# Kernel optimization log

Measured on AMD Instinct MI355X. Metric: run time of the kernel, lower is better.

Reference implementation:

```python
import jax, jax.numpy as jnp
import numpy as np

B, L, D, H, NLAYERS = 32, 2048, 1024, 16, 4
HD = D // H
NEG = -1e30


def setup_inputs() -> dict:
    key = jax.random.key(0)
    ks = jax.random.split(key, 12)
    tokens = jax.random.normal(ks[0], (B, L, D), dtype=jnp.float32)
    lengths = jax.random.randint(ks[1], (B,), 1, L + 1, dtype=jnp.int32)
    query_token = jax.random.normal(ks[2], (1, D), dtype=jnp.float32)
    s = 0.02
    Wq = jax.random.normal(ks[3], (NLAYERS, D, D), dtype=jnp.float32) * s
    Wk = jax.random.normal(ks[4], (NLAYERS, D, D), dtype=jnp.float32) * s
    Wv = jax.random.normal(ks[5], (NLAYERS, D, D), dtype=jnp.float32) * s
    Wo = jax.random.normal(ks[6], (NLAYERS, D, D), dtype=jnp.float32) * s
    bq = jnp.zeros((NLAYERS, D), jnp.float32)
    bk = jnp.zeros((NLAYERS, D), jnp.float32)
    bv = jnp.zeros((NLAYERS, D), jnp.float32)
    bo = jnp.zeros((NLAYERS, D), jnp.float32)
    gamma = jnp.ones((NLAYERS, D), jnp.float32)
    beta = jnp.zeros((NLAYERS, D), jnp.float32)
    return dict(tokens=tokens, lengths=lengths, query_token=query_token,
                Wq=Wq, bq=bq, Wk=Wk, bk=bk, Wv=Wv, bv=bv, Wo=Wo, bo=bo,
                gamma=gamma, beta=beta)


def _layernorm(x, g, b):
    mu = jnp.mean(x, axis=-1, keepdims=True)
    var = jnp.mean(jnp.square(x - mu), axis=-1, keepdims=True)
    return (x - mu) * jax.lax.rsqrt(var + 1e-5) * g + b


def reference(tokens, lengths, query_token, Wq, bq, Wk, bk, Wv, bv, Wo, bo, gamma, beta):
    # valid[b, l] = True where token l exists (inverse of key_padding_mask)
    valid = jnp.arange(L)[None, :] < lengths[:, None]            # [B, L]
    scale = 1.0 / jnp.sqrt(jnp.float32(HD))
    # zero out padded positions like the torch padded buffer (math-neutral)
    toks = tokens * valid[:, :, None].astype(tokens.dtype)       # [B, L, D]
    q = jnp.broadcast_to(query_token[None], (B, 1, D))           # [B, 1, D]
    for i in range(NLAYERS):
        qh = (q @ Wq[i] + bq[i]).reshape(B, 1, H, HD)            # [B, 1, H, hd]
        kh = (toks @ Wk[i] + bk[i]).reshape(B, L, H, HD)         # [B, L, H, hd]
        vh = (toks @ Wv[i] + bv[i]).reshape(B, L, H, HD)
        scores = jnp.einsum('bqhd,bkhd->bhqk', qh, kh) * scale   # [B, H, 1, L]
        scores = jnp.where(valid[:, None, None, :], scores, NEG)
        attn = jax.nn.softmax(scores, axis=-1)
        out = jnp.einsum('bhqk,bkhd->bqhd', attn, vh).reshape(B, 1, D)
        out = out @ Wo[i] + bo[i]
        q = _layernorm(out, gamma[i], beta[i])
    return q[:, 0, :]                                            # [B, D]
```

## Files before the change

### kernel.cpp

```cpp
#include <hip/hip_runtime.h>
#include <hip/hip_bf16.h>
#include <cstdint>
#include <cstddef>

#define BB 32
#define LL 2048
#define DD 1024
#define HH 16
#define HDIM 64
#define NL 4
#define NCHUNK 8
#define CHUNK 256
#define NEGINF -1e30f
#define PKS 16

typedef __attribute__((ext_vector_type(8))) short bf16x8;
typedef __attribute__((ext_vector_type(4))) float f32x4;

__device__ __forceinline__ unsigned short f2b(float x) {
    union { float f; unsigned int u; } v; v.f = x;
    unsigned int r = (v.u + 0x7FFFu + ((v.u >> 16) & 1u)) >> 16;
    return (unsigned short)r;
}
__device__ __forceinline__ float b2f(unsigned short u) {
    union { unsigned int u; float f; } v; v.u = ((unsigned int)u) << 16;
    return v.f;
}

template<int SRC>
__global__ __launch_bounds__(512) void k_gemv(
        const float* __restrict__ parts_in, const float* __restrict__ bias_in,
        const unsigned short* __restrict__ ctx16, const float* __restrict__ m_p,
        const float* __restrict__ s_p,
        const float* __restrict__ W, float* __restrict__ outp) {
    constexpr int KL = DD / PKS;
    int bid = blockIdx.x, tid = threadIdx.x;
    int ct = bid & 15, ks = bid >> 4;
    int e0 = ks * KL;
    __shared__ float Xs[BB][KL];
    __shared__ float wgtS[BB][NCHUNK];
    __shared__ float mgS[BB], SgS[BB];
    if (SRC == 3) {
        if (tid < BB) {
            int b = tid; float m = NEGINF;
            for (int c8 = 0; c8 < NCHUNK; ++c8)
                m = fmaxf(m, m_p[(b * NCHUNK + c8) * HH + ct]);
            float S = 0.f;
            for (int c8 = 0; c8 < NCHUNK; ++c8)
                S += s_p[(b * NCHUNK + c8) * HH + ct] *
                     __expf(m_p[(b * NCHUNK + c8) * HH + ct] - m);
            mgS[b] = m; SgS[b] = S;
        }
        __syncthreads();
        if (tid < 256) {
            int b = tid >> 3, c8 = tid & 7;
            wgtS[b][c8] = __expf(m_p[(b * NCHUNK + c8) * HH + ct] - mgS[b]) / SgS[b];
        }
        __syncthreads();
    }
    {
        int b = tid >> 4, kq = tid & 15;
        int k = kq * 4;
        float x0, x1, x2, x3;
        if (SRC == 2) {
            const float4 bi = *(const float4*)&bias_in[e0 + k];
            x0 = bi.x; x1 = bi.y; x2 = bi.z; x3 = bi.w;
#pragma unroll
            for (int j2 = 0; j2 < PKS; ++j2) {
                const float4 v = *(const float4*)&parts_in[((size_t)(j2 * BB) + b) * DD + e0 + k];
                x0 += v.x; x1 += v.y; x2 += v.z; x3 += v.w;
            }
        } else {
            x0 = x1 = x2 = x3 = 0.f;
#pragma unroll
            for (int c8 = 0; c8 < NCHUNK; ++c8) {
                const ushort4 u = *(const ushort4*)&ctx16[(((size_t)(b * NCHUNK + c8)) * HH + ct) * DD + e0 + k];
                float wq = wgtS[b][c8];
                x0 += wq * b2f(u.x); x1 += wq * b2f(u.y);
                x2 += wq * b2f(u.z); x3 += wq * b2f(u.w);
            }
        }
        float4 xv = {x0, x1, x2, x3};
        *(float4*)&Xs[b][k] = xv;
    }
    __syncthreads();
    int col = tid & 63, bg = tid >> 6;
    int c = ct * 64 + col;
    float acc[4] = {0.f, 0.f, 0.f, 0.f};
    for (int k = 0; k < KL; k += 4) {
        float w0 = W[(size_t)(e0 + k) * DD + c];
        float w1 = W[(size_t)(e0 + k + 1) * DD + c];
        float w2 = W[(size_t)(e0 + k + 2) * DD + c];
        float w3 = W[(size_t)(e0 + k + 3) * DD + c];
#pragma unroll
        for (int bb = 0; bb < 4; ++bb) {
            const float4 xv = *(const float4*)&Xs[bg * 4 + bb][k];
            acc[bb] += xv.x * w0 + xv.y * w1 + xv.z * w2 + xv.w * w3;
        }
    }
#pragma unroll
    for (int bb = 0; bb < 4; ++bb)
        outp[((size_t)(ks * BB) + bg * 4 + bb) * DD + c] = acc[bb];
}

__global__ __launch_bounds__(1024) void k_statsF(const float* __restrict__ parts,
        const float* __restrict__ bo, const float* __restrict__ gamma,
        const float* __restrict__ beta, float* __restrict__ outp) {
    int b = blockIdx.x, c = threadIdx.x;
    float v = bo[c];
#pragma unroll
    for (int ks = 0; ks < PKS; ++ks)
        v += parts[((size_t)(ks * BB) + b) * DD + c];
    float s1 = v, s2 = v * v;
#pragma unroll
    for (int off = 32; off; off >>= 1) {
        s1 += __shfl_xor(s1, off);
        s2 += __shfl_xor(s2, off);
    }
    __shared__ float r1[16], r2[16];
    __shared__ float smu, srs;
    int w = c >> 6;
    if ((c & 63) == 0) { r1[w] = s1; r2[w] = s2; }
    __syncthreads();
    if (c == 0) {
        float a = 0.f, q = 0.f;
#pragma unroll
        for (int i = 0; i < 16; ++i) { a += r1[i]; q += r2[i]; }
        float mu = a / (float)DD, var = q / (float)DD - mu * mu;
        smu = mu; srs = rsqrtf(var + 1e-5f);
    }
    __syncthreads();
    outp[(size_t)b * DD + c] = (v - smu) * srs * gamma[c] + beta[c];
}

__global__ __launch_bounds__(512) void k_qnext(const float* __restrict__ op,
        const float* __restrict__ bo, const float* __restrict__ gamma,
        const float* __restrict__ beta, const float* __restrict__ Wq,
        const float* __restrict__ bq, float* __restrict__ qh) {
    int bid = blockIdx.x, tid = threadIdx.x;
    int ct = bid & 15, bp = bid >> 4;
    int b0 = bp * 2;
    __shared__ float Xr[2][DD];
    __shared__ float pr[8][2][64];
    __shared__ float r1[8], r2[8];
    __shared__ float smu[2], srs[2];
    {
        int bb = tid >> 8, c4 = tid & 255;
        int c = c4 * 4;
        float4 x = *(const float4*)&bo[c];
#pragma unroll
        for (int ks = 0; ks < PKS; ++ks) {
            const float4 v = *(const float4*)&op[((size_t)(ks * BB) + b0 + bb) * DD + c];
            x.x += v.x; x.y += v.y; x.z += v.z; x.w += v.w;
        }
        *(float4*)&Xr[bb][c] = x;
    }
    __syncthreads();
    {
        int bb = tid >> 8, l = tid & 255;
        const float4 x = *(const float4*)&Xr[bb][l * 4];
        float s1 = x.x + x.y + x.z + x.w;
        float s2 = x.x * x.x + x.y * x.y + x.z * x.z + x.w * x.w;
#pragma unroll
        for (int off = 32; off; off >>= 1) {
            s1 += __shfl_xor(s1, off);
            s2 += __shfl_xor(s2, off);
        }
        int w = tid >> 6;
        if ((tid & 63) == 0) { r1[w] = s1; r2[w] = s2; }
    }
    __syncthreads();
    if (tid < 2) {
        float a = r1[tid * 4] + r1[tid * 4 + 1] + r1[tid * 4 + 2] + r1[tid * 4 + 3];
        float q = r2[tid * 4] + r2[tid * 4 + 1] + r2[tid * 4 + 2] + r2[tid * 4 + 3];
        float mu = a / (float)DD, var = q / (float)DD - mu * mu;
        smu[tid] = mu; srs[tid] = rsqrtf(var + 1e-5f);
    }
    __syncthreads();
    {
        int c = tid & 63, ks8 = tid >> 6;
        float mu0 = smu[0], rs0 = srs[0], mu1 = smu[1], rs1 = srs[1];
        float acc0 = 0.f, acc1 = 0.f;
        int k0 = ks8 * 128;
        for (int k = k0; k < k0 + 128; ++k) {
            float g = gamma[k], be = beta[k];
            float w = Wq[(size_t)k * DD + ct * 64 + c];
            float x0 = (Xr[0][k] - mu0) * rs0 * g + be;
            float x1 = (Xr[1][k] - mu1) * rs1 * g + be;
            acc0 += x0 * w;
            acc1 += x1 * w;
        }
        pr[ks8][0][c] = acc0;
        pr[ks8][1][c] = acc1;
    }
    __syncthreads();
    if (tid < 128) {
        int bb = tid >> 6, c = tid & 63;
        float q = bq[ct * 64 + c];
#pragma unroll
        for (int j = 0; j < 8; ++j) q += pr[j][bb][c];
        qh[((size_t)(b0 + bb)) * DD + ct * 64 + c] = q;
    }
}

__global__ __launch_bounds__(256) void k_q0(const float* __restrict__ qt,
        const float* __restrict__ Wq, const float* __restrict__ bq,
        float* __restrict__ qh) {
    int ct = blockIdx.x, tid = threadIdx.x;
    __shared__ float pr[4][64];
    int c = tid & 63, ks4 = tid >> 6;
    float acc = 0.f;
    int k0 = ks4 * 256;
    for (int k = k0; k < k0 + 256; ++k)
        acc += qt[k] * Wq[(size_t)k * DD + ct * 64 + c];
    pr[ks4][c] = acc;
    __syncthreads();
    if (tid < 64) {
        float q = bq[ct * 64 + tid];
#pragma unroll
        for (int j = 0; j < 4; ++j) q += pr[j][tid];
        qh[ct * 64 + tid] = q;
    }
}

template<int BCAST>
__global__ __launch_bounds__(256) void k_wk(const float* __restrict__ qh,
        const float* __restrict__ Wk, const float* __restrict__ bk,
        unsigned short* __restrict__ wk16, float* __restrict__ sb) {
    int h = blockIdx.x >> 4, et = blockIdx.x & 15;
    int tid = threadIdx.x;
    __shared__ float qs[BB][HDIM + 1];
    for (int i = tid; i < BB * HDIM; i += 256) {
        int bb = i >> 6, d = i & 63;
        qs[bb][d] = qh[((size_t)(BCAST ? 0 : bb)) * DD + h * HDIM + d];
    }
    __syncthreads();
    int b = tid & 31, eo = tid >> 5;
    for (int k = 0; k < 8; ++k) {
        int e = et * 64 + eo * 8 + k;
        const float* wrow = Wk + (size_t)e * DD + h * HDIM;
        float acc = 0.f;
#pragma unroll
        for (int d = 0; d < HDIM; ++d) acc += qs[b][d] * wrow[d];
        wk16[((size_t)(b * HH + h)) * DD + e] = f2b(acc);
    }
    if (et == 0 && tid < BB) {
        float acc = 0.f;
#pragma unroll
        for (int d = 0; d < HDIM; ++d) acc += qs[tid][d] * bk[h * HDIM + d];
        sb[tid * HH + h] = acc;
    }
}

template<int MODE>
__global__ __launch_bounds__(1024) void k_attn(const float* __restrict__ toks,
        unsigned short* __restrict__ tcache,
        const int* __restrict__ lens, const unsigned short* __restrict__ wk16,
        const float* __restrict__ sb, unsigned short* __restrict__ ctx16,
        float* __restrict__ m_p, float* __restrict__ s_p) {
    int b = blockIdx.x >> 3, chunk = blockIdx.x & 7;
    int tid = threadIdx.x, lane = tid & 63, w = tid >> 6;
    int len = lens[b];
    int base = chunk * CHUNK;
    int pidx = (b * NCHUNK + chunk) * HH;
    if (base >= len) {
        if (tid < HH) { m_p[pidx + tid] = NEGINF; s_p[pidx + tid] = 0.f; }
        return;
    }
    int nv = min(CHUNK, len - base);

    __shared__ __align__(16) unsigned short Tr[32][1032];
    __shared__ float Sred[16][HH][34];
    __shared__ unsigned short Pt[HH][40];
    __shared__ float sm_m[HH], sm_s[HH], sm_c[HH];

    if (tid < HH) { sm_m[tid] = NEGINF; sm_s[tid] = 0.f; }

    int hq = lane & 15, qg = lane >> 4;
    const unsigned short* wkb = wk16 + ((size_t)(b * HH + hq)) * DD + w * 64 + 8 * qg;
    bf16x8 afr0 = *(const bf16x8*)(wkb);
    bf16x8 afr1 = *(const bf16x8*)(wkb + 32);
    f32x4 zer = {0.f, 0.f, 0.f, 0.f};
    f32x4 ctxacc[4] = {zer, zer, zer, zer};
    float sbh = (tid < 512) ? sb[b * HH + (tid >> 5)] : 0.f;
    int st = tid >> 7;
    int se = (tid & 127) * 8;
    const size_t rowbase = (size_t)(b * LL + base);
    __syncthreads();

    for (int g = 0; g < 8; ++g) {
        int t0 = g * 32;
        if (t0 >= nv) break;
        if (MODE == 2) {
            const unsigned short* srcr = tcache + (rowbase + t0) * DD;
#pragma unroll
            for (int p = 0; p < 4; ++p) {
                int t = p * 8 + st;
                bf16x8 v = *(const bf16x8*)(srcr + (size_t)t * DD + se);
                *(bf16x8*)&Tr[t][se] = v;
            }
        } else {
            const float* srcr = toks + (rowbase + t0) * DD;
#pragma unroll
            for (int p = 0; p < 4; ++p) {
                int t = p * 8 + st;
                const float* sp = srcr + (size_t)t * DD + se;
                float4 a0 = *(const float4*)sp;
                float4 a1 = *(const float4*)(sp + 4);
                bf16x8 v;
                v[0] = f2b(a0.x); v[1] = f2b(a0.y); v[2] = f2b(a0.z); v[3] = f2b(a0.w);
                v[4] = f2b(a1.x); v[5] = f2b(a1.y); v[6] = f2b(a1.z); v[7] = f2b(a1.w);
                *(bf16x8*)&Tr[t][se] = v;
                if (MODE == 1)
                    *(bf16x8*)(tcache + (rowbase + t0 + t) * DD + se) = v;
            }
        }
        __syncthreads();
        f32x4 s0 = zer, s1 = zer;
        {
            int eb = w * 64 + 8 * qg;
            s0 = __builtin_amdgcn_mfma_f32_16x16x32_bf16(afr0, *(const bf16x8*)&Tr[hq][eb], s0, 0, 0, 0);
            s0 = __builtin_amdgcn_mfma_f32_16x16x32_bf16(afr1, *(const bf16x8*)&Tr[hq][eb + 32], s0, 0, 0, 0);
            s1 = __builtin_amdgcn_mfma_f32_16x16x32_bf16(afr0, *(const bf16x8*)&Tr[16 + hq][eb], s1, 0, 0, 0);
            s1 = __builtin_amdgcn_mfma_f32_16x16x32_bf16(afr1, *(const bf16x8*)&Tr[16 + hq][eb + 32], s1, 0, 0, 0);
        }
#pragma unroll
        for (int r = 0; r < 4; ++r) {
            Sred[w][qg * 4 + r][hq] = s0[r];
            Sred[w][qg * 4 + r][16 + hq] = s1[r];
        }
        __syncthreads();
        if (tid < 512) {
            int h = tid >> 5, t = tid & 31;
            float s = 0.f;
#pragma unroll
            for (int ww = 0; ww < 16; ++ww) s += Sred[ww][h][t];
            s = (s + sbh) * 0.125f;
            bool valid = (t0 + t) < nv;
            if (!valid) s = NEGINF;
            float tm = s;
#pragma unroll
            for (int off = 16; off; off >>= 1) tm = fmaxf(tm, __shfl_xor(tm, off, 32));
            float oldm = sm_m[h];
            float newm = fmaxf(oldm, tm);
            float pv = valid ? __expf(s - newm) : 0.f;
            float ps = pv;
#pragma unroll
            for (int off = 16; off; off >>= 1) ps += __shfl_xor(ps, off, 32);
            if (t == 0) {
                float corr = __expf(oldm - newm);
                sm_c[h] = corr;
                sm_m[h] = newm;
                sm_s[h] = sm_s[h] * corr + ps;
            }
            Pt[h][t] = f2b(pv);
        }
        __syncthreads();
        {
            float cr[4];
#pragma unroll
            for (int r = 0; r < 4; ++r) cr[r] = sm_c[qg * 4 + r];
            bf16x8 pafr;
            ushort4 pa0 = *(const ushort4*)&Pt[hq][8 * qg];
            ushort4 pa1 = *(const ushort4*)&Pt[hq][8 * qg + 4];
            pafr[0] = pa0.x; pafr[1] = pa0.y; pafr[2] = pa0.z; pafr[3] = pa0.w;
            pafr[4] = pa1.x; pafr[5] = pa1.y; pafr[6] = pa1.z; pafr[7] = pa1.w;
#pragma unroll
            for (int et = 0; et < 4; ++et) {
#pragma unroll
                for (int r = 0; r < 4; ++r) ctxacc[et][r] *= cr[r];
                bf16x8 bfr;
                int ec = w * 64 + et * 16 + hq;
#pragma unroll
                for (int i = 0; i < 8; ++i) bfr[i] = (short)Tr[8 * qg + i][ec];
                ctxacc[et] = __builtin_amdgcn_mfma_f32_16x16x32_bf16(pafr, bfr, ctxacc[et], 0, 0, 0);
            }
        }
        __syncthreads();
    }
    if (tid < HH) { m_p[pidx + tid] = sm_m[tid]; s_p[pidx + tid] = sm_s[tid]; }
#pragma unroll
    for (int et = 0; et < 4; ++et)
#pragma unroll
        for (int r = 0; r < 4; ++r) {
            int h = qg * 4 + r, e = w * 64 + et * 16 + hq;
            ctx16[((size_t)pidx + h) * DD + e] = f2b(ctxacc[et][r]);
        }
}

extern "C" void kernel_launch(void* const* d_in, const int* in_sizes, int n_in,
                              void* d_out, int out_size, void* d_ws, size_t ws_size,
                              hipStream_t stream) {
    const float* toks  = (const float*)d_in[0];
    const int*   lens  = (const int*)d_in[1];
    const float* qt    = (const float*)d_in[2];
    const float* Wq    = (const float*)d_in[3];
    const float* bq    = (const float*)d_in[4];
    const float* Wk    = (const float*)d_in[5];
    const float* bk    = (const float*)d_in[6];
    const float* Wv    = (const float*)d_in[7];
    const float* bv    = (const float*)d_in[8];
    const float* Wo    = (const float*)d_in[9];
    const float* bo    = (const float*)d_in[10];
    const float* gamma = (const float*)d_in[11];
    const float* beta  = (const float*)d_in[12];
    float* out = (float*)d_out;
    float* ws  = (float*)d_ws;

    unsigned short* ctx16 = (unsigned short*)ws;
    float* m_p   = ws + 2097152;
    float* s_p   = ws + 2101248;
    float* pvp   = ws + 2105344;
    float* op    = ws + 2629632;
    float* qh    = ws + 3153920;
    float* sbuf  = ws + 3186688;
    unsigned short* wk16 = (unsigned short*)(ws + 3187200);
    const size_t base_floats = 3449344;
    unsigned short* tcache = (unsigned short*)(ws + base_floats);
    const size_t need_cache = base_floats * 4 + (size_t)BB * LL * DD * 2;
    const bool use_cache = (ws_size >= need_cache);

    k_q0<<<16, 256, 0, stream>>>(qt, Wq, bq, qh);
    k_wk<1><<<256, 256, 0, stream>>>(qh, Wk, bk, wk16, sbuf);

    for (int i = 0; i < NL; ++i) {
        if (use_cache) {
            if (i == 0)
                k_attn<1><<<256, 1024, 0, stream>>>(toks, tcache, lens, wk16,
                        sbuf, ctx16, m_p, s_p);
            else
                k_attn<2><<<256, 1024, 0, stream>>>(toks, tcache, lens, wk16,
                        sbuf, ctx16, m_p, s_p);
        } else {
            k_attn<0><<<256, 1024, 0, stream>>>(toks, tcache, lens, wk16,
                    sbuf, ctx16, m_p, s_p);
        }
        const float* Wv_i = Wv + (size_t)i * DD * DD;
        const float* Wo_i = Wo + (size_t)i * DD * DD;
        k_gemv<3><<<256, 512, 0, stream>>>(nullptr, nullptr, ctx16, m_p, s_p,
                Wv_i, pvp);
        k_gemv<2><<<256, 512, 0, stream>>>(pvp, bv + i * DD, nullptr, nullptr,
                nullptr, Wo_i, op);
        if (i == NL - 1) {
            k_statsF<<<32, 1024, 0, stream>>>(op, bo + i * DD, gamma + i * DD,
                    beta + i * DD, out);
        } else {
            k_qnext<<<256, 512, 0, stream>>>(op, bo + i * DD, gamma + i * DD,
                    beta + i * DD, Wq + (size_t)(i + 1) * DD * DD,
                    bq + (i + 1) * DD, qh);
            k_wk<0><<<256, 256, 0, stream>>>(qh, Wk + (size_t)(i + 1) * DD * DD,
                    bk + (i + 1) * DD, wk16, sbuf);
        }
    }
}
```

Measured before the change: 338.5 us.

## Double-buffer token tiles in attention kernel and halve block size to 512 threads

The attention kernel now prefetches the next 32-token tile into registers while computing on the current tile, then writes it into a second LDS buffer, so global loads overlap with the MFMA and softmax work. Blocks shrink from 16 to 8 waves, and each wave now covers 128 embedding columns, doubling its score and context MFMAs. This cuts the number of barriers per tile and the partial-sum reduction width. In exchange, register pressure rises (16 float4 or 8 bf16x8 prefetch registers plus 8 accumulators), and there are fewer threads available to hide latency.

```diff
diff --git a/kernel.cpp b/kernel.cpp
--- a/kernel.cpp
+++ b/kernel.cpp
@@ -253,7 +253,7 @@
 }
 
 template<int MODE>
-__global__ __launch_bounds__(1024) void k_attn(const float* __restrict__ toks,
+__global__ __launch_bounds__(512) void k_attn(const float* __restrict__ toks,
         unsigned short* __restrict__ tcache,
         const int* __restrict__ lens, const unsigned short* __restrict__ wk16,
         const float* __restrict__ sb, unsigned short* __restrict__ ctx16,
@@ -268,61 +268,101 @@
         return;
     }
     int nv = min(CHUNK, len - base);
-
-    __shared__ __align__(16) unsigned short Tr[32][1032];
-    __shared__ float Sred[16][HH][34];
+    int ng = (nv + 31) >> 5;
+
+    __shared__ __align__(16) unsigned short Tr[2][32][1032];
+    __shared__ float Sred[8][HH][34];
     __shared__ unsigned short Pt[HH][40];
     __shared__ float sm_m[HH], sm_s[HH], sm_c[HH];
 
     if (tid < HH) { sm_m[tid] = NEGINF; sm_s[tid] = 0.f; }
 
     int hq = lane & 15, qg = lane >> 4;
-    const unsigned short* wkb = wk16 + ((size_t)(b * HH + hq)) * DD + w * 64 + 8 * qg;
+    const unsigned short* wkb = wk16 + ((size_t)(b * HH + hq)) * DD + w * 128 + 8 * qg;
     bf16x8 afr0 = *(const bf16x8*)(wkb);
     bf16x8 afr1 = *(const bf16x8*)(wkb + 32);
+    bf16x8 afr2 = *(const bf16x8*)(wkb + 64);
+    bf16x8 afr3 = *(const bf16x8*)(wkb + 96);
     f32x4 zer = {0.f, 0.f, 0.f, 0.f};
-    f32x4 ctxacc[4] = {zer, zer, zer, zer};
-    float sbh = (tid < 512) ? sb[b * HH + (tid >> 5)] : 0.f;
-    int st = tid >> 7;
-    int se = (tid & 127) * 8;
+    f32x4 ctxacc[8] = {zer, zer, zer, zer, zer, zer, zer, zer};
+    float sbh = sb[b * HH + (tid >> 5)];
+    int st = tid >> 6;
+    int se = (lane) * 16;
     const size_t rowbase = (size_t)(b * LL + base);
-    __syncthreads();
-
-    for (int g = 0; g < 8; ++g) {
+
+    float4 pa[16];
+    bf16x8 pc[8];
+
+    auto LOADR = [&](int g) {
+        if (MODE == 2) {
+            const unsigned short* s0p = tcache + (rowbase + g * 32) * DD + se;
+#pragma unroll
+            for (int p = 0; p < 4; ++p) {
+                const unsigned short* sp = s0p + (size_t)(p * 8 + st) * DD;
+                pc[2 * p]     = *(const bf16x8*)sp;
+                pc[2 * p + 1] = *(const bf16x8*)(sp + 8);
+            }
+        } else {
+            const float* s0p = toks + (rowbase + g * 32) * DD + se;
+#pragma unroll
+            for (int p = 0; p < 4; ++p) {
+                const float* sp = s0p + (size_t)(p * 8 + st) * DD;
+                pa[4 * p]     = *(const float4*)sp;
+                pa[4 * p + 1] = *(const float4*)(sp + 4);
+                pa[4 * p + 2] = *(const float4*)(sp + 8);
+                pa[4 * p + 3] = *(const float4*)(sp + 12);
+            }
+        }
+    };
+    auto WRITE = [&](int buf, int g) {
+        if (MODE == 2) {
+#pragma unroll
+            for (int p = 0; p < 4; ++p) {
+                *(bf16x8*)&Tr[buf][p * 8 + st][se]     = pc[2 * p];
+                *(bf16x8*)&Tr[buf][p * 8 + st][se + 8] = pc[2 * p + 1];
+            }
+        } else {
+#pragma unroll
+            for (int p = 0; p < 4; ++p) {
+                bf16x8 v0, v1;
+                v0[0] = f2b(pa[4 * p].x);     v0[1] = f2b(pa[4 * p].y);
+                v0[2] = f2b(pa[4 * p].z);     v0[3] = f2b(pa[4 * p].w);
+                v0[4] = f2b(pa[4 * p + 1].x); v0[5] = f2b(pa[4 * p + 1].y);
+                v0[6] = f2b(pa[4 * p + 1].z); v0[7] = f2b(pa[4 * p + 1].w);
+                v1[0] = f2b(pa[4 * p + 2].x); v1[1] = f2b(pa[4 * p + 2].y);
+                v1[2] = f2b(pa[4 * p + 2].z); v1[3] = f2b(pa[4 * p + 2].w);
+                v1[4] = f2b(pa[4 * p + 3].x); v1[5] = f2b(pa[4 * p + 3].y);
+                v1[6] = f2b(pa[4 * p + 3].z); v1[7] = f2b(pa[4 * p + 3].w);
+                *(bf16x8*)&Tr[buf][p * 8 + st][se]     = v0;
+                *(bf16x8*)&Tr[buf][p * 8 + st][se + 8] = v1;
+                if (MODE == 1) {
+                    unsigned short* cp = tcache + (rowbase + g * 32 + p * 8 + st) * DD + se;
+                    *(bf16x8*)cp = v0;
+                    *(bf16x8*)(cp + 8) = v1;
+                }
+            }
+        }
+    };
+
+    LOADR(0);
+    WRITE(0, 0);
+    __syncthreads();
+
+    for (int g = 0; g < ng; ++g) {
+        int cur = g & 1;
         int t0 = g * 32;
-        if (t0 >= nv) break;
-        if (MODE == 2) {
-            const unsigned short* srcr = tcache + (rowbase + t0) * DD;
-#pragma unroll
-            for (int p = 0; p < 4; ++p) {
-                int t = p * 8 + st;
-                bf16x8 v = *(const bf16x8*)(srcr + (size_t)t * DD + se);
-                *(bf16x8*)&Tr[t][se] = v;
-            }
-        } else {
-            const float* srcr = toks + (rowbase + t0) * DD;
-#pragma unroll
-            for (int p = 0; p < 4; ++p) {
-                int t = p * 8 + st;
-                const float* sp = srcr + (size_t)t * DD + se;
-                float4 a0 = *(const float4*)sp;
-                float4 a1 = *(const float4*)(sp + 4);
-                bf16x8 v;
-                v[0] = f2b(a0.x); v[1] = f2b(a0.y); v[2] = f2b(a0.z); v[3] = f2b(a0.w);
-                v[4] = f2b(a1.x); v[5] = f2b(a1.y); v[6] = f2b(a1.z); v[7] = f2b(a1.w);
-                *(bf16x8*)&Tr[t][se] = v;
-                if (MODE == 1)
-                    *(bf16x8*)(tcache + (rowbase + t0 + t) * DD + se) = v;
-            }
-        }
-        __syncthreads();
+        if (g + 1 < ng) LOADR(g + 1);
         f32x4 s0 = zer, s1 = zer;
         {
-            int eb = w * 64 + 8 * qg;
-            s0 = __builtin_amdgcn_mfma_f32_16x16x32_bf16(afr0, *(const bf16x8*)&Tr[hq][eb], s0, 0, 0, 0);
-            s0 = __builtin_amdgcn_mfma_f32_16x16x32_bf16(afr1, *(const bf16x8*)&Tr[hq][eb + 32], s0, 0, 0, 0);
-            s1 = __builtin_amdgcn_mfma_f32_16x16x32_bf16(afr0, *(const bf16x8*)&Tr[16 + hq][eb], s1, 0, 0, 0);
-            s1 = __builtin_amdgcn_mfma_f32_16x16x32_bf16(afr1, *(const bf16x8*)&Tr[16 + hq][eb + 32], s1, 0, 0, 0);
+            int eb = w * 128 + 8 * qg;
+            s0 = __builtin_amdgcn_mfma_f32_16x16x32_bf16(afr0, *(const bf16x8*)&Tr[cur][hq][eb], s0, 0, 0, 0);
+            s0 = __builtin_amdgcn_mfma_f32_16x16x32_bf16(afr1, *(const bf16x8*)&Tr[cur][hq][eb + 32], s0, 0, 0, 0);
+            s0 = __builtin_amdgcn_mfma_f32_16x16x32_bf16(afr2, *(const bf16x8*)&Tr[cur][hq][eb + 64], s0, 0, 0, 0);
+            s0 = __builtin_amdgcn_mfma_f32_16x16x32_bf16(afr3, *(const bf16x8*)&Tr[cur][hq][eb + 96], s0, 0, 0, 0);
+            s1 = __builtin_amdgcn_mfma_f32_16x16x32_bf16(afr0, *(const bf16x8*)&Tr[cur][16 + hq][eb], s1, 0, 0, 0);
+            s1 = __builtin_amdgcn_mfma_f32_16x16x32_bf16(afr1, *(const bf16x8*)&Tr[cur][16 + hq][eb + 32], s1, 0, 0, 0);
+            s1 = __builtin_amdgcn_mfma_f32_16x16x32_bf16(afr2, *(const bf16x8*)&Tr[cur][16 + hq][eb + 64], s1, 0, 0, 0);
+            s1 = __builtin_amdgcn_mfma_f32_16x16x32_bf16(afr3, *(const bf16x8*)&Tr[cur][16 + hq][eb + 96], s1, 0, 0, 0);
         }
 #pragma unroll
         for (int r = 0; r < 4; ++r) {
@@ -330,11 +370,11 @@
             Sred[w][qg * 4 + r][16 + hq] = s1[r];
         }
         __syncthreads();
-        if (tid < 512) {
+        {
             int h = tid >> 5, t = tid & 31;
             float s = 0.f;
 #pragma unroll
-            for (int ww = 0; ww < 16; ++ww) s += Sred[ww][h][t];
+            for (int ww = 0; ww < 8; ++ww) s += Sred[ww][h][t];
             s = (s + sbh) * 0.125f;
             bool valid = (t0 + t) < nv;
             if (!valid) s = NEGINF;
@@ -366,24 +406,25 @@
             pafr[0] = pa0.x; pafr[1] = pa0.y; pafr[2] = pa0.z; pafr[3] = pa0.w;
             pafr[4] = pa1.x; pafr[5] = pa1.y; pafr[6] = pa1.z; pafr[7] = pa1.w;
 #pragma unroll
-            for (int et = 0; et < 4; ++et) {
+            for (int et = 0; et < 8; ++et) {
 #pragma unroll
                 for (int r = 0; r < 4; ++r) ctxacc[et][r] *= cr[r];
                 bf16x8 bfr;
-                int ec = w * 64 + et * 16 + hq;
-#pragma unroll
-                for (int i = 0; i < 8; ++i) bfr[i] = (short)Tr[8 * qg + i][ec];
+                int ec = w * 128 + et * 16 + hq;
+#pragma unroll
+                for (int i = 0; i < 8; ++i) bfr[i] = (short)Tr[cur][8 * qg + i][ec];
                 ctxacc[et] = __builtin_amdgcn_mfma_f32_16x16x32_bf16(pafr, bfr, ctxacc[et], 0, 0, 0);
             }
         }
+        if (g + 1 < ng) WRITE(cur ^ 1, g + 1);
         __syncthreads();
     }
     if (tid < HH) { m_p[pidx + tid] = sm_m[tid]; s_p[pidx + tid] = sm_s[tid]; }
 #pragma unroll
-    for (int et = 0; et < 4; ++et)
+    for (int et = 0; et < 8; ++et)
 #pragma unroll
         for (int r = 0; r < 4; ++r) {
-            int h = qg * 4 + r, e = w * 64 + et * 16 + hq;
+            int h = qg * 4 + r, e = w * 128 + et * 16 + hq;
             ctx16[((size_t)pidx + h) * DD + e] = f2b(ctxacc[et][r]);
         }
 }
@@ -426,13 +467,13 @@
     for (int i = 0; i < NL; ++i) {
         if (use_cache) {
             if (i == 0)
-                k_attn<1><<<256, 1024, 0, stream>>>(toks, tcache, lens, wk16,
+                k_attn<1><<<256, 512, 0, stream>>>(toks, tcache, lens, wk16,
                         sbuf, ctx16, m_p, s_p);
             else
-                k_attn<2><<<256, 1024, 0, stream>>>(toks, tcache, lens, wk16,
+                k_attn<2><<<256, 512, 0, stream>>>(toks, tcache, lens, wk16,
                         sbuf, ctx16, m_p, s_p);
         } else {
-            k_attn<0><<<256, 1024, 0, stream>>>(toks, tcache, lens, wk16,
+            k_attn<0><<<256, 512, 0, stream>>>(toks, tcache, lens, wk16,
                     sbuf, ctx16, m_p, s_p);
         }
         const float* Wv_i = Wv + (size_t)i * DD * DD;
```

After: 337.8 us. About the same (-0.2%).

## Halve attention block to 512 threads with wider per-wave work and bf16 score reduction

Applied to the files above, without the earlier changes.

The attention kernel now launches 512 threads (8 waves) per block instead of 1024. Each wave covers 128 feature columns, holds twice the key fragments and context accumulators, and loads 16 elements per thread. Partial scores are now stored in shared memory as bf16 rather than fp32, which halves the reduction traffic but costs precision in the score sums. The loop count is computed up front instead of breaking early, and the launch bounds hint at 4 blocks per CU, though shared memory use may still cap residency.

```diff
diff --git a/kernel.cpp b/kernel.cpp
--- a/kernel.cpp
+++ b/kernel.cpp
@@ -253,7 +253,7 @@
 }
 
 template<int MODE>
-__global__ __launch_bounds__(1024) void k_attn(const float* __restrict__ toks,
+__global__ __launch_bounds__(512, 4) void k_attn(const float* __restrict__ toks,
         unsigned short* __restrict__ tcache,
         const int* __restrict__ lens, const unsigned short* __restrict__ wk16,
         const float* __restrict__ sb, unsigned short* __restrict__ ctx16,
@@ -268,73 +268,86 @@
         return;
     }
     int nv = min(CHUNK, len - base);
+    int ng = (nv + 31) >> 5;
 
     __shared__ __align__(16) unsigned short Tr[32][1032];
-    __shared__ float Sred[16][HH][34];
+    __shared__ unsigned short SredH[8][HH][34];
     __shared__ unsigned short Pt[HH][40];
     __shared__ float sm_m[HH], sm_s[HH], sm_c[HH];
 
     if (tid < HH) { sm_m[tid] = NEGINF; sm_s[tid] = 0.f; }
 
     int hq = lane & 15, qg = lane >> 4;
-    const unsigned short* wkb = wk16 + ((size_t)(b * HH + hq)) * DD + w * 64 + 8 * qg;
+    const unsigned short* wkb = wk16 + ((size_t)(b * HH + hq)) * DD + w * 128 + 8 * qg;
     bf16x8 afr0 = *(const bf16x8*)(wkb);
     bf16x8 afr1 = *(const bf16x8*)(wkb + 32);
+    bf16x8 afr2 = *(const bf16x8*)(wkb + 64);
+    bf16x8 afr3 = *(const bf16x8*)(wkb + 96);
     f32x4 zer = {0.f, 0.f, 0.f, 0.f};
-    f32x4 ctxacc[4] = {zer, zer, zer, zer};
-    float sbh = (tid < 512) ? sb[b * HH + (tid >> 5)] : 0.f;
-    int st = tid >> 7;
-    int se = (tid & 127) * 8;
+    f32x4 ctxacc[8] = {zer, zer, zer, zer, zer, zer, zer, zer};
+    float sbh = sb[b * HH + (tid >> 5)];
+    int st = tid >> 6;
+    int se = lane * 16;
     const size_t rowbase = (size_t)(b * LL + base);
     __syncthreads();
 
-    for (int g = 0; g < 8; ++g) {
+    for (int g = 0; g < ng; ++g) {
         int t0 = g * 32;
-        if (t0 >= nv) break;
         if (MODE == 2) {
-            const unsigned short* srcr = tcache + (rowbase + t0) * DD;
+            const unsigned short* s0p = tcache + (rowbase + t0) * DD + se;
 #pragma unroll
             for (int p = 0; p < 4; ++p) {
-                int t = p * 8 + st;
-                bf16x8 v = *(const bf16x8*)(srcr + (size_t)t * DD + se);
-                *(bf16x8*)&Tr[t][se] = v;
+                const unsigned short* sp = s0p + (size_t)(p * 8 + st) * DD;
+                *(bf16x8*)&Tr[p * 8 + st][se]     = *(const bf16x8*)sp;
+                *(bf16x8*)&Tr[p * 8 + st][se + 8] = *(const bf16x8*)(sp + 8);
             }
         } else {
-            const float* srcr = toks + (rowbase + t0) * DD;
+            const float* s0p = toks + (rowbase + t0) * DD + se;
 #pragma unroll
             for (int p = 0; p < 4; ++p) {
-                int t = p * 8 + st;
-                const float* sp = srcr + (size_t)t * DD + se;
+                const float* sp = s0p + (size_t)(p * 8 + st) * DD;
                 float4 a0 = *(const float4*)sp;
                 float4 a1 = *(const float4*)(sp + 4);
-                bf16x8 v;
-                v[0] = f2b(a0.x); v[1] = f2b(a0.y); v[2] = f2b(a0.z); v[3] = f2b(a0.w);
-                v[4] = f2b(a1.x); v[5] = f2b(a1.y); v[6] = f2b(a1.z); v[7] = f2b(a1.w);
-                *(bf16x8*)&Tr[t][se] = v;
-                if (MODE == 1)
-                    *(bf16x8*)(tcache + (rowbase + t0 + t) * DD + se) = v;
+                float4 a2 = *(const float4*)(sp + 8);
+                float4 a3 = *(const float4*)(sp + 12);
+                bf16x8 v0, v1;
+                v0[0] = f2b(a0.x); v0[1] = f2b(a0.y); v0[2] = f2b(a0.z); v0[3] = f2b(a0.w);
+                v0[4] = f2b(a1.x); v0[5] = f2b(a1.y); v0[6] = f2b(a1.z); v0[7] = f2b(a1.w);
+                v1[0] = f2b(a2.x); v1[1] = f2b(a2.y); v1[2] = f2b(a2.z); v1[3] = f2b(a2.w);
+                v1[4] = f2b(a3.x); v1[5] = f2b(a3.y); v1[6] = f2b(a3.z); v1[7] = f2b(a3.w);
+                *(bf16x8*)&Tr[p * 8 + st][se]     = v0;
+                *(bf16x8*)&Tr[p * 8 + st][se + 8] = v1;
+                if (MODE == 1) {
+                    unsigned short* cp = tcache + (rowbase + t0 + p * 8 + st) * DD + se;
+                    *(bf16x8*)cp = v0;
+                    *(bf16x8*)(cp + 8) = v1;
+                }
             }
         }
         __syncthreads();
         f32x4 s0 = zer, s1 = zer;
         {
-            int eb = w * 64 + 8 * qg;
+            int eb = w * 128 + 8 * qg;
             s0 = __builtin_amdgcn_mfma_f32_16x16x32_bf16(afr0, *(const bf16x8*)&Tr[hq][eb], s0, 0, 0, 0);
             s0 = __builtin_amdgcn_mfma_f32_16x16x32_bf16(afr1, *(const bf16x8*)&Tr[hq][eb + 32], s0, 0, 0, 0);
+            s0 = __builtin_amdgcn_mfma_f32_16x16x32_bf16(afr2, *(const bf16x8*)&Tr[hq][eb + 64], s0, 0, 0, 0);
+            s0 = __builtin_amdgcn_mfma_f32_16x16x32_bf16(afr3, *(const bf16x8*)&Tr[hq][eb + 96], s0, 0, 0, 0);
             s1 = __builtin_amdgcn_mfma_f32_16x16x32_bf16(afr0, *(const bf16x8*)&Tr[16 + hq][eb], s1, 0, 0, 0);
             s1 = __builtin_amdgcn_mfma_f32_16x16x32_bf16(afr1, *(const bf16x8*)&Tr[16 + hq][eb + 32], s1, 0, 0, 0);
+            s1 = __builtin_amdgcn_mfma_f32_16x16x32_bf16(afr2, *(const bf16x8*)&Tr[16 + hq][eb + 64], s1, 0, 0, 0);
+            s1 = __builtin_amdgcn_mfma_f32_16x16x32_bf16(afr3, *(const bf16x8*)&Tr[16 + hq][eb + 96], s1, 0, 0, 0);
         }
 #pragma unroll
         for (int r = 0; r < 4; ++r) {
-            Sred[w][qg * 4 + r][hq] = s0[r];
-            Sred[w][qg * 4 + r][16 + hq] = s1[r];
-        }
-        __syncthreads();
-        if (tid < 512) {
+            SredH[w][qg * 4 + r][hq] = f2b(s0[r]);
+            SredH[w][qg * 4 + r][16 + hq] = f2b(s1[r]);
+        }
+        __syncthreads();
+        {
             int h = tid >> 5, t = tid & 31;
             float s = 0.f;
 #pragma unroll
-            for (int ww = 0; ww < 16; ++ww) s += Sred[ww][h][t];
+            for (int ww = 0; ww < 8; ++ww) s += b2f(SredH[ww][h][t]);
             s = (s + sbh) * 0.125f;
             bool valid = (t0 + t) < nv;
             if (!valid) s = NEGINF;
@@ -366,11 +379,11 @@
             pafr[0] = pa0.x; pafr[1] = pa0.y; pafr[2] = pa0.z; pafr[3] = pa0.w;
             pafr[4] = pa1.x; pafr[5] = pa1.y; pafr[6] = pa1.z; pafr[7] = pa1.w;
 #pragma unroll
-            for (int et = 0; et < 4; ++et) {
+            for (int et = 0; et < 8; ++et) {
 #pragma unroll
                 for (int r = 0; r < 4; ++r) ctxacc[et][r] *= cr[r];
                 bf16x8 bfr;
-                int ec = w * 64 + et * 16 + hq;
+                int ec = w * 128 + et * 16 + hq;
 #pragma unroll
                 for (int i = 0; i < 8; ++i) bfr[i] = (short)Tr[8 * qg + i][ec];
                 ctxacc[et] = __builtin_amdgcn_mfma_f32_16x16x32_bf16(pafr, bfr, ctxacc[et], 0, 0, 0);
@@ -380,10 +393,10 @@
     }
     if (tid < HH) { m_p[pidx + tid] = sm_m[tid]; s_p[pidx + tid] = sm_s[tid]; }
 #pragma unroll
-    for (int et = 0; et < 4; ++et)
+    for (int et = 0; et < 8; ++et)
 #pragma unroll
         for (int r = 0; r < 4; ++r) {
-            int h = qg * 4 + r, e = w * 64 + et * 16 + hq;
+            int h = qg * 4 + r, e = w * 128 + et * 16 + hq;
             ctx16[((size_t)pidx + h) * DD + e] = f2b(ctxacc[et][r]);
         }
 }
@@ -426,13 +439,13 @@
     for (int i = 0; i < NL; ++i) {
         if (use_cache) {
             if (i == 0)
-                k_attn<1><<<256, 1024, 0, stream>>>(toks, tcache, lens, wk16,
+                k_attn<1><<<256, 512, 0, stream>>>(toks, tcache, lens, wk16,
                         sbuf, ctx16, m_p, s_p);
             else
-                k_attn<2><<<256, 1024, 0, stream>>>(toks, tcache, lens, wk16,
+                k_attn<2><<<256, 512, 0, stream>>>(toks, tcache, lens, wk16,
                         sbuf, ctx16, m_p, s_p);
         } else {
-            k_attn<0><<<256, 1024, 0, stream>>>(toks, tcache, lens, wk16,
+            k_attn<0><<<256, 512, 0, stream>>>(toks, tcache, lens, wk16,
                     sbuf, ctx16, m_p, s_p);
         }
         const float* Wv_i = Wv + (size_t)i * DD * DD;
```

After: 345.1 us. About the same (+2.0%).
